# Kernel optimization log

Hardware: AMD Instinct MI355X
Metric: run time of the kernel (lower is better)

The kernel has to match this reference:

```python
import jax, jax.numpy as jnp
import numpy as np

K = 3          # kernel size
STRIDE = 1
PAD = 1
DIL = 1
K2 = K * K     # number of sampling locations per output pixel


def conv2d(x, w, b, stride=STRIDE, pad=PAD, dil=DIL):
    # x: [B,C,H,W], w: [O,I,K,K], b: [O]
    out = jax.lax.conv_general_dilated(
        x, w, window_strides=(stride, stride),
        padding=[(pad, pad), (pad, pad)], rhs_dilation=(dil, dil),
        dimension_numbers=('NCHW', 'OIHW', 'NCHW'))
    return out + b[None, :, None, None]


def bilinear_sample(x, sy, sx):
    # x: [B,C,H,W]; sy, sx: [B,K2,Ho,Wo] float sampling coords (y, x)
    # zero padding outside the image (torchvision deform_conv2d semantics)
    B, C, H, W = x.shape
    x_flat = x.reshape(B, C, H * W)

    y0 = jnp.floor(sy)
    x0 = jnp.floor(sx)
    wy1 = sy - y0  # frac weights
    wx1 = sx - x0
    wy0 = 1.0 - wy1
    wx0 = 1.0 - wx1

    def gather(yi, xi):
        valid = ((yi >= 0) & (yi < H) & (xi >= 0) & (xi < W)).astype(x.dtype)
        yc = jnp.clip(yi, 0, H - 1).astype(jnp.int32)
        xc = jnp.clip(xi, 0, W - 1).astype(jnp.int32)
        idx = (yc * W + xc).reshape(B, 1, -1)  # [B,1,K2*Ho*Wo]
        v = jnp.take_along_axis(x_flat, idx, axis=2)  # [B,C,K2*Ho*Wo]
        v = v.reshape(B, C, *yi.shape[1:])            # [B,C,K2,Ho,Wo]
        return v * valid[:, None]

    out = (gather(y0,     x0    ) * (wy0 * wx0)[:, None]
         + gather(y0,     x0 + 1) * (wy0 * wx1)[:, None]
         + gather(y0 + 1, x0    ) * (wy1 * wx0)[:, None]
         + gather(y0 + 1, x0 + 1) * (wy1 * wx1)[:, None])
    return out  # [B,C,K2,Ho,Wo]


def setup_inputs() -> dict:
    key = jax.random.key(0)
    ks = jax.random.split(key, 6)
    B, C, H, W = 4, 64, 128, 128
    Cout = 64
    x = jax.random.normal(ks[0], (B, C, H, W), jnp.float32)
    # offset conv: 2*K2 output channels; small init -> small offsets (realistic)
    w_off = jax.random.normal(ks[1], (2 * K2, C, K, K), jnp.float32) * 0.01
    b_off = jnp.zeros((2 * K2,), jnp.float32)
    # mask conv: K2 output channels, sigmoid activation
    w_mask = jax.random.normal(ks[2], (K2, C, K, K), jnp.float32) * 0.01
    b_mask = jnp.zeros((K2,), jnp.float32)  # mask_init_bias = 0
    # main deformable conv weights
    w = jax.random.normal(ks[3], (Cout, C, K, K), jnp.float32) * (1.0 / np.sqrt(C * K2))
    b = jnp.zeros((Cout,), jnp.float32)
    return {"x": x, "w_off": w_off, "b_off": b_off,
            "w_mask": w_mask, "b_mask": b_mask, "w": w, "b": b}


def reference(x, w_off, b_off, w_mask, b_mask, w, b):
    B, C, H, W = x.shape
    Cout = w.shape[0]

    offset = conv2d(x, w_off, b_off)                    # [B,2*K2,Ho,Wo]
    mask = jax.nn.sigmoid(conv2d(x, w_mask, b_mask))    # [B,K2,Ho,Wo]
    Ho, Wo = offset.shape[2], offset.shape[3]

    off = offset.reshape(B, K2, 2, Ho, Wo)
    dy, dx = off[:, :, 0], off[:, :, 1]                 # torchvision layout: (y,x) pairs

    ki = (jnp.arange(K2) // K).astype(jnp.float32)      # kernel row index
    kj = (jnp.arange(K2) % K).astype(jnp.float32)       # kernel col index
    base_y = (jnp.arange(Ho, dtype=jnp.float32) * STRIDE - PAD)[None, :, None] \
             + (ki * DIL)[:, None, None]                # [K2,Ho,1]
    base_x = (jnp.arange(Wo, dtype=jnp.float32) * STRIDE - PAD)[None, None, :] \
             + (kj * DIL)[:, None, None]                # [K2,1,Wo]

    sy = base_y[None] + dy                              # [B,K2,Ho,Wo]
    sx = base_x[None] + dx

    sampled = bilinear_sample(x, sy, sx) * mask[:, None]  # [B,C,K2,Ho,Wo]
    out = jnp.einsum('bckhw,ock->bohw', sampled, w.reshape(Cout, C, K2))
    return out + b[None, :, None, None]
```

## Files before the change

kernel.cpp:

```cpp
#include <hip/hip_runtime.h>
#include <math.h>

typedef __attribute__((ext_vector_type(8))) short short8;
typedef __attribute__((ext_vector_type(4))) float f32x4;
typedef unsigned short ushort_t;
typedef unsigned int uint_t;

#define HH 128
#define WW 128
#define CC 64
#define HWp 16384

__device__ inline ushort_t f2bf(float f) {
    uint_t u = __float_as_uint(f);
    uint_t r = (u + 0x7FFFu + ((u >> 16) & 1u)) >> 16;
    return (ushort_t)r;
}
__device__ inline float blo(uint_t u) { return __uint_as_float(u << 16); }
__device__ inline float bhi(uint_t u) { return __uint_as_float(u & 0xFFFF0000u); }
__device__ inline short8 bc8(uint4 v) { return __builtin_bit_cast(short8, v); }

__global__ __launch_bounds__(256) void k_pack(const float* __restrict__ w_off,
        const float* __restrict__ w_mask, const float* __restrict__ w,
        ushort_t* __restrict__ wpom, ushort_t* __restrict__ wpm) {
    int idx = blockIdx.x * 256 + threadIdx.x;
    if (idx < 18432) {
        int e = idx;
        int j = e & 7, l = (e >> 3) & 63, mf = (e >> 9) & 1, ks = e >> 10;
        int ch = mf * 16 + (l & 15);
        int k = ks * 32 + ((l >> 4) << 3) + j;
        int c = k & 63, kk = k >> 6;
        float v = 0.f;
        if (ch < 18) v = w_off[(ch * CC + c) * 9 + kk];
        else if (ch < 27) v = w_mask[((ch - 18) * CC + c) * 9 + kk];
        wpom[idx] = f2bf(v);
    } else if (idx < 18432 + 36864) {
        int e = idx - 18432;
        int j = e & 7, l = (e >> 3) & 63, mf = (e >> 9) & 3, ks = e >> 11;
        int o = mf * 16 + (l & 15);
        int k = ks * 32 + ((l >> 4) << 3) + j;
        int c = k & 63, kk = k >> 6;
        wpm[e] = f2bf(w[(o * CC + c) * 9 + kk]);
    }
}

__global__ __launch_bounds__(256) void k_transpose_x(const float* __restrict__ x,
                                                     ushort_t* __restrict__ xtb) {
    __shared__ float tile[64][65];
    int bid = blockIdx.x;
    int xs = (bid & 1) * 64;
    int y  = (bid >> 1) & 127;
    int b  = bid >> 8;
    int t = threadIdx.x, lane = t & 63, g = t >> 6;
#pragma unroll
    for (int i = 0; i < 16; ++i) {
        int c = i * 4 + g;
        tile[c][lane] = x[(((size_t)b * CC + c) * HH + y) * WW + xs + lane];
    }
    __syncthreads();
#pragma unroll
    for (int i = 0; i < 16; ++i) {
        int xx = i * 4 + g;
        xtb[(((size_t)b * HH + y) * WW + xs + xx) * CC + lane] = f2bf(tile[lane][xx]);
    }
}

__global__ __launch_bounds__(512, 4) void k_conv_om(const ushort_t* __restrict__ xtb,
        const uint4* __restrict__ wpom, const float* __restrict__ b_off,
        const float* __restrict__ b_mask, float* __restrict__ om) {
    __shared__ ushort_t xrow[3 * 132 * 64];
    int blk = blockIdx.x;
    int y = blk & 127, b = blk >> 7;
    int t = threadIdx.x;

    for (int ky = 0; ky < 3; ++ky) {
        int yy = y + ky - 1;
        bool ok = (yy >= 0) && (yy < HH);
#pragma unroll
        for (int i = 0; i < 2; ++i) {
            int t2 = i * 512 + t;
            int colr = t2 >> 3;
            int c0 = (t2 & 7) * 8;
            uint4 v = make_uint4(0u, 0u, 0u, 0u);
            if (ok) v = *(const uint4*)&xtb[(((size_t)b * HWp) + yy * WW + colr) * CC + c0];
            int col = colr + 1;
            int idx = ((ky * 132 + col) * 64 + c0) ^ ((col & 7) << 3);
            *(uint4*)&xrow[idx] = v;
        }
    }
    if (t < 48) {
        int ky = t >> 4, cs = (t >> 3) & 1, chn = t & 7;
        int col = cs ? 129 : 0;
        int idx = ((ky * 132 + col) * 64 + chn * 8) ^ ((col & 7) << 3);
        *(uint4*)&xrow[idx] = make_uint4(0u, 0u, 0u, 0u);
    }
    __syncthreads();

    int lane = t & 63, w = t >> 6;
    int lm = lane & 15, lg = lane >> 4;
    int px = w * 16 + lm;
    f32x4 acc[2] = {};
#pragma unroll
    for (int ks = 0; ks < 18; ++ks) {
        int kk = ks >> 1;
        int kyy = kk / 3, kxx = kk % 3;
        int c0 = (ks & 1) * 32 + lg * 8;
        short8 a0 = bc8(wpom[(ks * 2 + 0) * 64 + lane]);
        short8 a1 = bc8(wpom[(ks * 2 + 1) * 64 + lane]);
        int col = px + kxx;
        int idx = ((kyy * 132 + col) * 64 + c0) ^ ((col & 7) << 3);
        short8 bf = *(const short8*)&xrow[idx];
        acc[0] = __builtin_amdgcn_mfma_f32_16x16x32_bf16(a0, bf, acc[0], 0, 0, 0);
        acc[1] = __builtin_amdgcn_mfma_f32_16x16x32_bf16(a1, bf, acc[1], 0, 0, 0);
    }
#pragma unroll
    for (int mf = 0; mf < 2; ++mf)
#pragma unroll
        for (int r = 0; r < 4; ++r) {
            int ch = mf * 16 + lg * 4 + r;
            if (ch < 27) {
                float v = acc[mf][r] + (ch < 18 ? b_off[ch] : b_mask[ch - 18]);
                if (ch >= 18) v = 1.f / (1.f + __expf(-v));
                om[(((size_t)b * 27 + ch) << 14) + (y << 7) + px] = v;
            }
        }
}

__global__ __launch_bounds__(512, 4) void k_fused(const ushort_t* __restrict__ xtb,
        const float* __restrict__ om, const uint4* __restrict__ wpm,
        const float* __restrict__ bias, float* __restrict__ out) {
    __shared__ __align__(16) ushort_t sm[32 * 576];
    __shared__ __align__(16) float prm[288 * 8];
    int blk = blockIdx.x;
    int b = blk >> 9, rem = blk & 511;
    int y = rem >> 2, xs = (rem & 3) * 32;
    int t = threadIdx.x, lane = t & 63, w = t >> 6;
    const char* xbB = (const char*)xtb + ((size_t)b << 21);
    const float* omb = om + (((size_t)b * 27) << 14) + (y << 7) + xs;

    if (t < 288) {
        int k = t >> 5, px = t & 31;
        int ki = k / 3, kj = k - ki * 3;
        int x = xs + px;
        float dy = omb[((2 * k) << 14) + px];
        float dx = omb[((2 * k + 1) << 14) + px];
        float m  = omb[((18 + k) << 14) + px];
        float sy = (float)(y - 1 + ki) + dy;
        float sx = (float)(x - 1 + kj) + dx;
        float fy = floorf(sy), fx = floorf(sx);
        float wy1 = sy - fy, wx1 = sx - fx;
        float wy0 = 1.f - wy1, wx0 = 1.f - wx1;
        int iy0 = (int)fy, ix0 = (int)fx;
        int iy1 = iy0 + 1, ix1 = ix0 + 1;
        bool vy0 = (iy0 >= 0) & (iy0 < HH);
        bool vy1 = (iy1 >= 0) & (iy1 < HH);
        float wyr0 = vy0 ? wy0 : (vy1 ? wy1 : 0.f);
        int   ry0  = vy0 ? iy0 : (vy1 ? iy1 : 0);
        float wyr1 = (vy0 & vy1) ? wy1 : 0.f;
        int   ry1  = min(max(iy1, 0), HH - 1);
        int bx = min(max(ix0, 0), WW - 2);
        float wxh0 = (bx == ix0) ? wx0 : ((bx == ix1) ? wx1 : 0.f);
        float wxh1 = (bx + 1 == ix1) ? wx1 : ((bx + 1 == ix0) ? wx0 : 0.f);
        int s = px * 9 + k;
        float* pp = prm + s * 8;
        pp[0] = m * wyr0 * wxh0;
        pp[1] = m * wyr0 * wxh1;
        pp[2] = m * wyr1 * wxh0;
        pp[3] = m * wyr1 * wxh1;
        pp[4] = __uint_as_float((uint_t)(((ry0 << 7) + bx) << 7));
        pp[5] = __uint_as_float((uint_t)(((ry1 << 7) + bx) << 7));
        pp[6] = __uint_as_float((uint_t)(px * 576 + k * 64));
        pp[7] = __uint_as_float((uint_t)(((px ^ k) & 7) << 3));
    }
    __syncthreads();

    {
        int g = lane & 15;
        int q = lane >> 4;
        int sbase = w * 36 + q;
        int g8 = g << 3;
#pragma unroll
        for (int i = 0; i < 9; ++i) {
            int s = sbase + i * 4;
            const float* pp = prm + s * 8;
            f32x4 wv  = *(const f32x4*)pp;
            f32x4 aux = *(const f32x4*)(pp + 4);
            uint_t aT = __float_as_uint(aux.x) + (uint_t)g8;
            uint_t aB = __float_as_uint(aux.y) + (uint_t)g8;
            uint2 tl = *(const uint2*)(xbB + aT);
            uint2 tr = *(const uint2*)(xbB + aT + 128);
            uint2 bl = *(const uint2*)(xbB + aB);
            uint2 br = *(const uint2*)(xbB + aB + 128);
            float s0 = wv.x*blo(tl.x) + wv.y*blo(tr.x) + wv.z*blo(bl.x) + wv.w*blo(br.x);
            float s1 = wv.x*bhi(tl.x) + wv.y*bhi(tr.x) + wv.z*bhi(bl.x) + wv.w*bhi(br.x);
            float s2 = wv.x*blo(tl.y) + wv.y*blo(tr.y) + wv.z*blo(bl.y) + wv.w*blo(br.y);
            float s3 = wv.x*bhi(tl.y) + wv.y*bhi(tr.y) + wv.z*bhi(bl.y) + wv.w*bhi(br.y);
            uint_t r01, r23;
            asm("v_cvt_pk_bf16_f32 %0, %1, %2" : "=v"(r01) : "v"(s0), "v"(s1));
            asm("v_cvt_pk_bf16_f32 %0, %1, %2" : "=v"(r23) : "v"(s2), "v"(s3));
            int widx = (int)((__float_as_uint(aux.z) + (uint_t)(g << 2)) ^ __float_as_uint(aux.w));
            *(uint2*)&sm[widx] = make_uint2(r01, r23);
        }
    }
    __syncthreads();

    int lm = lane & 15, lg = lane >> 4;
    int mf = w & 3, nh = w >> 2;
    int px_r = (nh << 4) + lm;
    f32x4 acc = {};
#pragma unroll
    for (int ks = 0; ks < 18; ++ks) {
        short8 af = bc8(wpm[((ks << 2) + mf) * 64 + lane]);
        int bidx = (px_r * 576 + (ks << 5) + (lg << 3)) ^ (((px_r ^ (ks >> 1)) & 7) << 3);
        short8 bf = *(const short8*)&sm[bidx];
        acc = __builtin_amdgcn_mfma_f32_16x16x32_bf16(af, bf, acc, 0, 0, 0);
    }
#pragma unroll
    for (int r = 0; r < 4; ++r) {
        int o = (mf << 4) + (lg << 2) + r;
        out[(((size_t)b * 64 + o) << 14) + (y << 7) + xs + px_r] = acc[r] + bias[o];
    }
}

extern "C" void kernel_launch(void* const* d_in, const int* in_sizes, int n_in,
                              void* d_out, int out_size, void* d_ws, size_t ws_size,
                              hipStream_t stream) {
    const float* x      = (const float*)d_in[0];
    const float* w_off  = (const float*)d_in[1];
    const float* b_off  = (const float*)d_in[2];
    const float* w_mask = (const float*)d_in[3];
    const float* b_mask = (const float*)d_in[4];
    const float* w      = (const float*)d_in[5];
    const float* bias   = (const float*)d_in[6];
    float* out = (float*)d_out;

    char* ws = (char*)d_ws;
    ushort_t* xtb  = (ushort_t*)(ws);
    float*    om   = (float*)(ws + 8388608);
    ushort_t* wpom = (ushort_t*)(ws + 15466496);
    ushort_t* wpm  = (ushort_t*)(ws + 15503360);

    hipLaunchKernelGGL(k_pack, dim3(216), dim3(256), 0, stream,
                       w_off, w_mask, w, wpom, wpm);
    hipLaunchKernelGGL(k_transpose_x, dim3(1024), dim3(256), 0, stream, x, xtb);
    hipLaunchKernelGGL(k_conv_om, dim3(512), dim3(512), 0, stream,
                       xtb, (const uint4*)wpom, b_off, b_mask, om);
    hipLaunchKernelGGL(k_fused, dim3(2048), dim3(512), 0, stream,
                       xtb, om, (const uint4*)wpm, bias, out);
}
```

Measured before the change: 59.27 us.

## Widen gathers, vectorize transpose, split offset conv blocks, raise fused occupancy

The transpose kernel now reads float4 vectors and writes packed bf16 pairs. The offset/mask conv is split into half-row blocks of 256 threads, which gives more blocks and a smaller LDS footprint. In the fused kernel, each lane now gathers 16-byte corner vectors covering 8 channels instead of 8-byte ones, and the next sample's gathers are software-pipelined with double buffering. The occupancy hint for the fused kernel is raised to 6 blocks. Together these aim to cut memory instruction count and latency, at the cost of more registers and some redundant clamped work for the tail samples.

```diff
diff --git a/kernel.cpp b/kernel.cpp
--- a/kernel.cpp
+++ b/kernel.cpp
@@ -19,6 +19,22 @@
 __device__ inline float blo(uint_t u) { return __uint_as_float(u << 16); }
 __device__ inline float bhi(uint_t u) { return __uint_as_float(u & 0xFFFF0000u); }
 __device__ inline short8 bc8(uint4 v) { return __builtin_bit_cast(short8, v); }
+
+__device__ inline uint_t pk2(f32x4 wv, uint_t a, uint_t b, uint_t c, uint_t d) {
+    float lo = wv.x * blo(a) + wv.y * blo(b) + wv.z * blo(c) + wv.w * blo(d);
+    float hi = wv.x * bhi(a) + wv.y * bhi(b) + wv.z * bhi(c) + wv.w * bhi(d);
+    uint_t r;
+    asm("v_cvt_pk_bf16_f32 %0, %1, %2" : "=v"(r) : "v"(lo), "v"(hi));
+    return r;
+}
+__device__ inline short8 bilerp8(f32x4 wv, uint4 A, uint4 B, uint4 C, uint4 D) {
+    uint4 r;
+    r.x = pk2(wv, A.x, B.x, C.x, D.x);
+    r.y = pk2(wv, A.y, B.y, C.y, D.y);
+    r.z = pk2(wv, A.z, B.z, C.z, D.z);
+    r.w = pk2(wv, A.w, B.w, C.w, D.w);
+    return __builtin_bit_cast(short8, r);
+}
 
 __global__ __launch_bounds__(256) void k_pack(const float* __restrict__ w_off,
         const float* __restrict__ w_mask, const float* __restrict__ w,
@@ -46,59 +62,63 @@
 
 __global__ __launch_bounds__(256) void k_transpose_x(const float* __restrict__ x,
                                                      ushort_t* __restrict__ xtb) {
-    __shared__ float tile[64][65];
+    __shared__ __align__(16) float tile[64][68];
     int bid = blockIdx.x;
     int xs = (bid & 1) * 64;
     int y  = (bid >> 1) & 127;
     int b  = bid >> 8;
-    int t = threadIdx.x, lane = t & 63, g = t >> 6;
-#pragma unroll
-    for (int i = 0; i < 16; ++i) {
-        int c = i * 4 + g;
-        tile[c][lane] = x[(((size_t)b * CC + c) * HH + y) * WW + xs + lane];
-    }
-    __syncthreads();
-#pragma unroll
-    for (int i = 0; i < 16; ++i) {
-        int xx = i * 4 + g;
-        xtb[(((size_t)b * HH + y) * WW + xs + xx) * CC + lane] = f2bf(tile[lane][xx]);
-    }
-}
-
-__global__ __launch_bounds__(512, 4) void k_conv_om(const ushort_t* __restrict__ xtb,
+    int t = threadIdx.x;
+#pragma unroll
+    for (int i = 0; i < 4; ++i) {
+        int c  = i * 16 + (t >> 4);
+        int xl = (t & 15) << 2;
+        float4 v = *(const float4*)&x[(((size_t)b * CC + c) * HH + y) * WW + xs + xl];
+        *(float4*)&tile[c][xl] = v;
+    }
+    __syncthreads();
+#pragma unroll
+    for (int i = 0; i < 8; ++i) {
+        int pxl = i * 8 + (t >> 5);
+        int cp  = t & 31;
+        float v0 = tile[cp * 2][pxl], v1 = tile[cp * 2 + 1][pxl];
+        uint_t pk;
+        asm("v_cvt_pk_bf16_f32 %0, %1, %2" : "=v"(pk) : "v"(v0), "v"(v1));
+        *(uint_t*)&xtb[(((size_t)b * HH + y) * WW + xs + pxl) * CC + cp * 2] = pk;
+    }
+}
+
+__global__ __launch_bounds__(256, 4) void k_conv_om(const ushort_t* __restrict__ xtb,
         const uint4* __restrict__ wpom, const float* __restrict__ b_off,
         const float* __restrict__ b_mask, float* __restrict__ om) {
-    __shared__ ushort_t xrow[3 * 132 * 64];
+    __shared__ ushort_t xrow[3 * 68 * 64];
     int blk = blockIdx.x;
-    int y = blk & 127, b = blk >> 7;
+    int b = blk >> 8, rem = blk & 255;
+    int y = rem >> 1, xh = (rem & 1) * 64;
     int t = threadIdx.x;
 
     for (int ky = 0; ky < 3; ++ky) {
         int yy = y + ky - 1;
-        bool ok = (yy >= 0) && (yy < HH);
-#pragma unroll
-        for (int i = 0; i < 2; ++i) {
-            int t2 = i * 512 + t;
-            int colr = t2 >> 3;
-            int c0 = (t2 & 7) * 8;
-            uint4 v = make_uint4(0u, 0u, 0u, 0u);
-            if (ok) v = *(const uint4*)&xtb[(((size_t)b * HWp) + yy * WW + colr) * CC + c0];
-            int col = colr + 1;
-            int idx = ((ky * 132 + col) * 64 + c0) ^ ((col & 7) << 3);
-            *(uint4*)&xrow[idx] = v;
-        }
-    }
-    if (t < 48) {
-        int ky = t >> 4, cs = (t >> 3) & 1, chn = t & 7;
-        int col = cs ? 129 : 0;
-        int idx = ((ky * 132 + col) * 64 + chn * 8) ^ ((col & 7) << 3);
-        *(uint4*)&xrow[idx] = make_uint4(0u, 0u, 0u, 0u);
+        bool rok = (yy >= 0) && (yy < HH);
+#pragma unroll
+        for (int i = 0; i < 3; ++i) {
+            int t2 = i * 256 + t;
+            if (t2 < 528) {
+                int cl = t2 >> 3;
+                int c0 = (t2 & 7) * 8;
+                int xcoord = xh - 1 + cl;
+                bool ok = rok && (xcoord >= 0) && (xcoord < WW);
+                uint4 v = make_uint4(0u, 0u, 0u, 0u);
+                if (ok) v = *(const uint4*)&xtb[(((size_t)b * HWp) + yy * WW + xcoord) * CC + c0];
+                int idx = ((ky * 68 + cl) * 64 + c0) ^ ((cl & 7) << 3);
+                *(uint4*)&xrow[idx] = v;
+            }
+        }
     }
     __syncthreads();
 
     int lane = t & 63, w = t >> 6;
     int lm = lane & 15, lg = lane >> 4;
-    int px = w * 16 + lm;
+    int pxl = w * 16 + lm;
     f32x4 acc[2] = {};
 #pragma unroll
     for (int ks = 0; ks < 18; ++ks) {
@@ -107,12 +127,13 @@
         int c0 = (ks & 1) * 32 + lg * 8;
         short8 a0 = bc8(wpom[(ks * 2 + 0) * 64 + lane]);
         short8 a1 = bc8(wpom[(ks * 2 + 1) * 64 + lane]);
-        int col = px + kxx;
-        int idx = ((kyy * 132 + col) * 64 + c0) ^ ((col & 7) << 3);
+        int cl = pxl + kxx;
+        int idx = ((kyy * 68 + cl) * 64 + c0) ^ ((cl & 7) << 3);
         short8 bf = *(const short8*)&xrow[idx];
         acc[0] = __builtin_amdgcn_mfma_f32_16x16x32_bf16(a0, bf, acc[0], 0, 0, 0);
         acc[1] = __builtin_amdgcn_mfma_f32_16x16x32_bf16(a1, bf, acc[1], 0, 0, 0);
     }
+    int px = xh + pxl;
 #pragma unroll
     for (int mf = 0; mf < 2; ++mf)
 #pragma unroll
@@ -126,7 +147,7 @@
         }
 }
 
-__global__ __launch_bounds__(512, 4) void k_fused(const ushort_t* __restrict__ xtb,
+__global__ __launch_bounds__(512, 6) void k_fused(const ushort_t* __restrict__ xtb,
         const float* __restrict__ om, const uint4* __restrict__ wpm,
         const float* __restrict__ bias, float* __restrict__ out) {
     __shared__ __align__(16) ushort_t sm[32 * 576];
@@ -175,31 +196,37 @@
     __syncthreads();
 
     {
-        int g = lane & 15;
-        int q = lane >> 4;
-        int sbase = w * 36 + q;
-        int g8 = g << 3;
-#pragma unroll
-        for (int i = 0; i < 9; ++i) {
-            int s = sbase + i * 4;
-            const float* pp = prm + s * 8;
-            f32x4 wv  = *(const f32x4*)pp;
-            f32x4 aux = *(const f32x4*)(pp + 4);
-            uint_t aT = __float_as_uint(aux.x) + (uint_t)g8;
-            uint_t aB = __float_as_uint(aux.y) + (uint_t)g8;
-            uint2 tl = *(const uint2*)(xbB + aT);
-            uint2 tr = *(const uint2*)(xbB + aT + 128);
-            uint2 bl = *(const uint2*)(xbB + aB);
-            uint2 br = *(const uint2*)(xbB + aB + 128);
-            float s0 = wv.x*blo(tl.x) + wv.y*blo(tr.x) + wv.z*blo(bl.x) + wv.w*blo(br.x);
-            float s1 = wv.x*bhi(tl.x) + wv.y*bhi(tr.x) + wv.z*bhi(bl.x) + wv.w*bhi(br.x);
-            float s2 = wv.x*blo(tl.y) + wv.y*blo(tr.y) + wv.z*blo(bl.y) + wv.w*blo(br.y);
-            float s3 = wv.x*bhi(tl.y) + wv.y*bhi(tr.y) + wv.z*bhi(bl.y) + wv.w*bhi(br.y);
-            uint_t r01, r23;
-            asm("v_cvt_pk_bf16_f32 %0, %1, %2" : "=v"(r01) : "v"(s0), "v"(s1));
-            asm("v_cvt_pk_bf16_f32 %0, %1, %2" : "=v"(r23) : "v"(s2), "v"(s3));
-            int widx = (int)((__float_as_uint(aux.z) + (uint_t)(g << 2)) ^ __float_as_uint(aux.w));
-            *(uint2*)&sm[widx] = make_uint2(r01, r23);
+        int g = lane >> 3, j = lane & 7;
+        uint_t j16 = (uint_t)(j << 4);
+        uint_t jw  = (uint_t)(j << 3);
+        int s0 = w * 36 + g;
+        uint4 axv[5];
+#pragma unroll
+        for (int r = 0; r < 5; ++r) {
+            int s = s0 + r * 8; s = s > 287 ? 287 : s;
+            axv[r] = *(const uint4*)(prm + s * 8 + 4);
+        }
+        uint4 tlA, trA, blA, brA, tlB, trB, blB, brB;
+        {
+            uint_t aT = axv[0].x + j16, aB = axv[0].y + j16;
+            tlA = *(const uint4*)(xbB + aT);  trA = *(const uint4*)(xbB + aT + 128);
+            blA = *(const uint4*)(xbB + aB);  brA = *(const uint4*)(xbB + aB + 128);
+        }
+#pragma unroll
+        for (int r = 0; r < 5; ++r) {
+            if (r < 4) {
+                uint_t aT = axv[r + 1].x + j16, aB = axv[r + 1].y + j16;
+                tlB = *(const uint4*)(xbB + aT);  trB = *(const uint4*)(xbB + aT + 128);
+                blB = *(const uint4*)(xbB + aB);  brB = *(const uint4*)(xbB + aB + 128);
+            }
+            int s = s0 + r * 8; s = s > 287 ? 287 : s;
+            f32x4 wv = *(const f32x4*)(prm + s * 8);
+            short8 bf = bilerp8(wv, tlA, trA, blA, brA);
+            if (r < 4 || g < 4) {
+                uint_t widx = (axv[r].z + jw) ^ axv[r].w;
+                *(short8*)&sm[widx] = bf;
+            }
+            tlA = tlB; trA = trB; blA = blB; brA = brB;
         }
     }
     __syncthreads();
@@ -243,7 +270,7 @@
     hipLaunchKernelGGL(k_pack, dim3(216), dim3(256), 0, stream,
                        w_off, w_mask, w, wpom, wpm);
     hipLaunchKernelGGL(k_transpose_x, dim3(1024), dim3(256), 0, stream, x, xtb);
-    hipLaunchKernelGGL(k_conv_om, dim3(512), dim3(512), 0, stream,
+    hipLaunchKernelGGL(k_conv_om, dim3(1024), dim3(256), 0, stream,
                        xtb, (const uint4*)wpom, b_off, b_mask, om);
     hipLaunchKernelGGL(k_fused, dim3(2048), dim3(512), 0, stream,
                        xtb, om, (const uint4*)wpm, bias, out);
```

New measurement: 54.76 us. -7.6%, faster.
